# Kernel optimization log

Hardware: AMD Instinct MI355X
Metric: run time of the kernel (lower is better)

The kernel has to match this reference:

```python
import jax, jax.numpy as jnp
import numpy as np

B, L = 4096, 4096  # batch of spectra, spectrum length
MIN_W, MAX_W = 1024, 3072  # ragged overlap-window lengths


def setup_inputs() -> dict:
    key = jax.random.key(0)
    k1, k2, k3, k4, k5, k6 = jax.random.split(key, 6)
    fluctuate = jax.random.normal(k1, (B, 1, L), dtype=jnp.float32)
    ivar = jax.random.uniform(k2, (B, 1, L), dtype=jnp.float32)
    output = jax.random.normal(k3, (B, 1, L), dtype=jnp.float32)
    # per-sample window length and valid starts in both input and output
    lens = jax.random.randint(k4, (B,), MIN_W, MAX_W + 1)
    s_in = jax.random.randint(k5, (B,), 0, L - lens + 1)
    s_out = jax.random.randint(k6, (B,), 0, L - lens + 1)
    overlap_index = jnp.stack([s_in, s_in + lens, s_out, s_out + lens], axis=1).astype(jnp.int64)
    return {"fluctuate": fluctuate, "ivar": ivar, "output": output, "overlap_index": overlap_index}


def reference(fluctuate, ivar, output, overlap_index):
    # fluctuate/ivar: [B,1,L]; output: [B,1,Lo]; overlap_index: [B,4] = [s_in, e_in, s_out, e_out]
    Bn, _, Ln = fluctuate.shape
    Lo = output.shape[-1]
    s_in = overlap_index[:, 0]
    e_in = overlap_index[:, 1]
    s_out = overlap_index[:, 2]
    lens = e_in - s_in  # equal to e_out - s_out by construction

    j = jnp.arange(Ln)                           # [L] padded window positions
    mask = j[None, :] < lens[:, None]            # [B,L] valid positions
    idx_in = jnp.clip(s_in[:, None] + j[None, :], 0, Ln - 1)   # [B,L]
    idx_out = jnp.clip(s_out[:, None] + j[None, :], 0, Lo - 1)  # [B,L]

    x = jnp.take_along_axis(fluctuate[:, 0, :], idx_in, axis=1)
    w = jnp.take_along_axis(ivar[:, 0, :], idx_in, axis=1)
    y = jnp.take_along_axis(output[:, 0, :], idx_out, axis=1)

    sq = jnp.where(mask, (x - y) ** 2 * w, jnp.float32(0))
    per_sample = sq.sum(axis=1) / lens.astype(sq.dtype)  # mean over each ragged window
    return per_sample.mean()
```

## Files before the change

### kernel.cpp

```cpp
#include <hip/hip_runtime.h>

#define BLOCK 256

__global__ __launch_bounds__(BLOCK) void chi2_per_sample(
    const float* __restrict__ fluct,
    const float* __restrict__ ivar,
    const float* __restrict__ outp,
    const int*  __restrict__ ovl,
    float* __restrict__ partial,
    int L)
{
    const int b = blockIdx.x;
    const int s_in  = ovl[b * 4 + 0];
    const int e_in  = ovl[b * 4 + 1];
    const int s_out = ovl[b * 4 + 2];
    const int len   = e_in - s_in;

    const float* __restrict__ xp = fluct + (size_t)b * L + s_in;
    const float* __restrict__ wp = ivar  + (size_t)b * L + s_in;
    const float* __restrict__ yp = outp  + (size_t)b * L + s_out;

    float acc = 0.f;
    for (int j = threadIdx.x; j < len; j += BLOCK) {
        const float d = xp[j] - yp[j];
        acc = fmaf(d * d, wp[j], acc);
    }

    #pragma unroll
    for (int off = 32; off > 0; off >>= 1)
        acc += __shfl_down(acc, off, 64);

    __shared__ float sacc[BLOCK / 64];
    if ((threadIdx.x & 63) == 0) sacc[threadIdx.x >> 6] = acc;
    __syncthreads();

    if (threadIdx.x == 0) {
        float s = 0.f;
        #pragma unroll
        for (int i = 0; i < BLOCK / 64; ++i) s += sacc[i];
        partial[b] = s / (float)len;
    }
}

__global__ __launch_bounds__(BLOCK) void chi2_reduce_mean(
    const float* __restrict__ partial, float* __restrict__ out, int B)
{
    float acc = 0.f;
    for (int i = threadIdx.x; i < B; i += BLOCK) acc += partial[i];

    #pragma unroll
    for (int off = 32; off > 0; off >>= 1)
        acc += __shfl_down(acc, off, 64);

    __shared__ float sacc[BLOCK / 64];
    if ((threadIdx.x & 63) == 0) sacc[threadIdx.x >> 6] = acc;
    __syncthreads();

    if (threadIdx.x == 0) {
        float s = 0.f;
        #pragma unroll
        for (int i = 0; i < BLOCK / 64; ++i) s += sacc[i];
        out[0] = s / (float)B;
    }
}

extern "C" void kernel_launch(void* const* d_in, const int* in_sizes, int n_in,
                              void* d_out, int out_size, void* d_ws, size_t ws_size,
                              hipStream_t stream) {
    const float* fluct = (const float*)d_in[0];
    const float* ivar  = (const float*)d_in[1];
    const float* outp  = (const float*)d_in[2];
    const int*   ovl   = (const int*)d_in[3];

    const int B = in_sizes[3] / 4;
    const int L = in_sizes[0] / B;

    float* partial = (float*)d_ws;

    chi2_per_sample<<<B, BLOCK, 0, stream>>>(fluct, ivar, outp, ovl, partial, L);
    chi2_reduce_mean<<<1, BLOCK, 0, stream>>>(partial, (float*)d_out, B);
}
```

Baseline: 182.2 us.

## Map one wavefront per sample with vectorized float4 loads and unrolled accumulators

```diff
diff --git a/kernel.cpp b/kernel.cpp
--- a/kernel.cpp
+++ b/kernel.cpp
@@ -1,6 +1,9 @@
 #include <hip/hip_runtime.h>
 
 #define BLOCK 256
+
+typedef float f4a __attribute__((ext_vector_type(4)));
+typedef float f4u __attribute__((ext_vector_type(4), aligned(4)));
 
 __global__ __launch_bounds__(BLOCK) void chi2_per_sample(
     const float* __restrict__ fluct,
@@ -10,36 +13,83 @@
     float* __restrict__ partial,
     int L)
 {
-    const int b = blockIdx.x;
-    const int s_in  = ovl[b * 4 + 0];
-    const int e_in  = ovl[b * 4 + 1];
-    const int s_out = ovl[b * 4 + 2];
+    const int wave = (blockIdx.x * BLOCK + threadIdx.x) >> 6;
+    const int lane = threadIdx.x & 63;
+
+    const int s_in  = ovl[wave * 4 + 0];
+    const int e_in  = ovl[wave * 4 + 1];
+    const int s_out = ovl[wave * 4 + 2];
     const int len   = e_in - s_in;
 
-    const float* __restrict__ xp = fluct + (size_t)b * L + s_in;
-    const float* __restrict__ wp = ivar  + (size_t)b * L + s_in;
-    const float* __restrict__ yp = outp  + (size_t)b * L + s_out;
+    const float* __restrict__ xp = fluct + (size_t)wave * L + s_in;
+    const float* __restrict__ wp = ivar  + (size_t)wave * L + s_in;
+    const float* __restrict__ yp = outp  + (size_t)wave * L + s_out;
+
+    const int align = (4 - (s_in & 3)) & 3;
 
     float acc = 0.f;
-    for (int j = threadIdx.x; j < len; j += BLOCK) {
-        const float d = xp[j] - yp[j];
-        acc = fmaf(d * d, wp[j], acc);
+    if (lane < align) {
+        const float d = xp[lane] - yp[lane];
+        acc = fmaf(d * d, wp[lane], acc);
     }
+
+    const int n4 = (len - align) >> 2;
+    const f4a* __restrict__ x4 = reinterpret_cast<const f4a*>(xp + align);
+    const f4a* __restrict__ w4 = reinterpret_cast<const f4a*>(wp + align);
+    const float* __restrict__ yb = yp + align;
+
+    float a0 = 0.f, a1 = 0.f, a2 = 0.f, a3 = 0.f;
+    int c = lane;
+    for (; c + 192 < n4; c += 256) {
+        const f4a xv0 = x4[c];
+        const f4a xv1 = x4[c +  64];
+        const f4a xv2 = x4[c + 128];
+        const f4a xv3 = x4[c + 192];
+        const f4u yv0 = *reinterpret_cast<const f4u*>(yb + 4 * c);
+        const f4u yv1 = *reinterpret_cast<const f4u*>(yb + 4 * (c +  64));
+        const f4u yv2 = *reinterpret_cast<const f4u*>(yb + 4 * (c + 128));
+        const f4u yv3 = *reinterpret_cast<const f4u*>(yb + 4 * (c + 192));
+        const f4a wv0 = w4[c];
+        const f4a wv1 = w4[c +  64];
+        const f4a wv2 = w4[c + 128];
+        const f4a wv3 = w4[c + 192];
+        #pragma unroll
+        for (int e = 0; e < 4; ++e) {
+            const float d0 = xv0[e] - yv0[e];
+            const float d1 = xv1[e] - yv1[e];
+            const float d2 = xv2[e] - yv2[e];
+            const float d3 = xv3[e] - yv3[e];
+            a0 = fmaf(d0 * d0, wv0[e], a0);
+            a1 = fmaf(d1 * d1, wv1[e], a1);
+            a2 = fmaf(d2 * d2, wv2[e], a2);
+            a3 = fmaf(d3 * d3, wv3[e], a3);
+        }
+    }
+    for (; c < n4; c += 64) {
+        const f4a xv = x4[c];
+        const f4u yv = *reinterpret_cast<const f4u*>(yb + 4 * c);
+        const f4a wv = w4[c];
+        #pragma unroll
+        for (int e = 0; e < 4; ++e) {
+            const float d = xv[e] - yv[e];
+            a0 = fmaf(d * d, wv[e], a0);
+        }
+    }
+    const int done = align + (n4 << 2);
+    const int rem  = len - done;
+    if (lane < rem) {
+        const float d = xp[done + lane] - yp[done + lane];
+        acc = fmaf(d * d, wp[done + lane], acc);
+    }
+
+    acc += (a0 + a1) + (a2 + a3);
 
     #pragma unroll
     for (int off = 32; off > 0; off >>= 1)
         acc += __shfl_down(acc, off, 64);
 
-    __shared__ float sacc[BLOCK / 64];
-    if ((threadIdx.x & 63) == 0) sacc[threadIdx.x >> 6] = acc;
-    __syncthreads();
-
-    if (threadIdx.x == 0) {
-        float s = 0.f;
-        #pragma unroll
-        for (int i = 0; i < BLOCK / 64; ++i) s += sacc[i];
-        partial[b] = s / (float)len;
-    }
+    if (lane == 0)
+        partial[wave] = acc / (float)len;
 }
 
 __global__ __launch_bounds__(BLOCK) void chi2_reduce_mean(
@@ -77,6 +127,8 @@
 
     float* partial = (float*)d_ws;
 
-    chi2_per_sample<<<B, BLOCK, 0, stream>>>(fluct, ivar, outp, ovl, partial, L);
+    const int waves_per_block = BLOCK / 64;
+    chi2_per_sample<<<B / waves_per_block, BLOCK, 0, stream>>>(
+        fluct, ivar, outp, ovl, partial, L);
     chi2_reduce_mean<<<1, BLOCK, 0, stream>>>(partial, (float*)d_out, B);
 }
```

New measurement: 182.4 us. About the same (+0.1%).

## Fuse per-sample and mean reductions with vectorized loads and two waves per sample

Applied to the files above, without the earlier changes.

```diff
diff --git a/kernel.cpp b/kernel.cpp
--- a/kernel.cpp
+++ b/kernel.cpp
@@ -2,65 +2,81 @@
 
 #define BLOCK 256
 
-__global__ __launch_bounds__(BLOCK) void chi2_per_sample(
+typedef float f4u __attribute__((ext_vector_type(4), aligned(4)));
+
+__global__ __launch_bounds__(BLOCK, 8) void chi2_fused(
     const float* __restrict__ fluct,
     const float* __restrict__ ivar,
     const float* __restrict__ outp,
     const int*  __restrict__ ovl,
-    float* __restrict__ partial,
-    int L)
+    float* __restrict__ out,
+    int L, float inv_B)
 {
-    const int b = blockIdx.x;
-    const int s_in  = ovl[b * 4 + 0];
-    const int e_in  = ovl[b * 4 + 1];
-    const int s_out = ovl[b * 4 + 2];
-    const int len   = e_in - s_in;
+    const int gwave = (blockIdx.x * BLOCK + threadIdx.x) >> 6;
+    const int lane  = threadIdx.x & 63;
+    const int b     = gwave >> 1;
+    const int h     = gwave & 1;
+
+    const int4 o   = reinterpret_cast<const int4*>(ovl)[b];
+    const int s_in = o.x, e_in = o.y, s_out = o.z;
+    const int len  = e_in - s_in;
 
     const float* __restrict__ xp = fluct + (size_t)b * L + s_in;
     const float* __restrict__ wp = ivar  + (size_t)b * L + s_in;
     const float* __restrict__ yp = outp  + (size_t)b * L + s_out;
 
-    float acc = 0.f;
-    for (int j = threadIdx.x; j < len; j += BLOCK) {
-        const float d = xp[j] - yp[j];
-        acc = fmaf(d * d, wp[j], acc);
+    const int n4 = len >> 2;
+
+    float a0 = 0.f, a1 = 0.f;
+    int c = lane + (h << 6);
+    for (; c + 128 < n4; c += 256) {
+        const f4u xv0 = *reinterpret_cast<const f4u*>(xp + 4 * c);
+        const f4u xv1 = *reinterpret_cast<const f4u*>(xp + 4 * (c + 128));
+        const f4u yv0 = *reinterpret_cast<const f4u*>(yp + 4 * c);
+        const f4u yv1 = *reinterpret_cast<const f4u*>(yp + 4 * (c + 128));
+        const f4u wv0 = *reinterpret_cast<const f4u*>(wp + 4 * c);
+        const f4u wv1 = *reinterpret_cast<const f4u*>(wp + 4 * (c + 128));
+        #pragma unroll
+        for (int e = 0; e < 4; ++e) {
+            const float d0 = xv0[e] - yv0[e];
+            const float d1 = xv1[e] - yv1[e];
+            a0 = fmaf(d0 * d0, wv0[e], a0);
+            a1 = fmaf(d1 * d1, wv1[e], a1);
+        }
     }
+    for (; c < n4; c += 128) {
+        const f4u xv = *reinterpret_cast<const f4u*>(xp + 4 * c);
+        const f4u yv = *reinterpret_cast<const f4u*>(yp + 4 * c);
+        const f4u wv = *reinterpret_cast<const f4u*>(wp + 4 * c);
+        #pragma unroll
+        for (int e = 0; e < 4; ++e) {
+            const float d = xv[e] - yv[e];
+            a0 = fmaf(d * d, wv[e], a0);
+        }
+    }
+    if (h) {
+        const int done = n4 << 2;
+        if (lane < (len & 3)) {
+            const float d = xp[done + lane] - yp[done + lane];
+            a0 = fmaf(d * d, wp[done + lane], a0);
+        }
+    }
+
+    float acc = a0 + a1;
 
     #pragma unroll
     for (int off = 32; off > 0; off >>= 1)
         acc += __shfl_down(acc, off, 64);
 
     __shared__ float sacc[BLOCK / 64];
-    if ((threadIdx.x & 63) == 0) sacc[threadIdx.x >> 6] = acc;
+    if (lane == 0) sacc[threadIdx.x >> 6] = (acc / (float)len) * inv_B;
     __syncthreads();
 
     if (threadIdx.x == 0) {
         float s = 0.f;
         #pragma unroll
         for (int i = 0; i < BLOCK / 64; ++i) s += sacc[i];
-        partial[b] = s / (float)len;
-    }
-}
-
-__global__ __launch_bounds__(BLOCK) void chi2_reduce_mean(
-    const float* __restrict__ partial, float* __restrict__ out, int B)
-{
-    float acc = 0.f;
-    for (int i = threadIdx.x; i < B; i += BLOCK) acc += partial[i];
-
-    #pragma unroll
-    for (int off = 32; off > 0; off >>= 1)
-        acc += __shfl_down(acc, off, 64);
-
-    __shared__ float sacc[BLOCK / 64];
-    if ((threadIdx.x & 63) == 0) sacc[threadIdx.x >> 6] = acc;
-    __syncthreads();
-
-    if (threadIdx.x == 0) {
-        float s = 0.f;
-        #pragma unroll
-        for (int i = 0; i < BLOCK / 64; ++i) s += sacc[i];
-        out[0] = s / (float)B;
+        atomicAdd(out, s);
     }
 }
 
@@ -75,8 +91,10 @@
     const int B = in_sizes[3] / 4;
     const int L = in_sizes[0] / B;
 
-    float* partial = (float*)d_ws;
+    hipMemsetAsync(d_out, 0, sizeof(float) * out_size, stream);
 
-    chi2_per_sample<<<B, BLOCK, 0, stream>>>(fluct, ivar, outp, ovl, partial, L);
-    chi2_reduce_mean<<<1, BLOCK, 0, stream>>>(partial, (float*)d_out, B);
+    const int waves_per_block = BLOCK / 64;
+    const int total_waves = B * 2;
+    chi2_fused<<<total_waves / waves_per_block, BLOCK, 0, stream>>>(
+        fluct, ivar, outp, ovl, (float*)d_out, L, 1.0f / (float)B);
 }
```

Result: slower. 186.3 us (+2.3%).
